# Kernel optimization log

Hardware: AMD Instinct MI355X
Metric: run time of the kernel (lower is better)

## Reference

```python
import jax, jax.numpy as jnp
import numpy as np

B, L, D, H = 2, 2048, 1024, 16
DH = D // H


def setup_inputs() -> dict:
    key = jax.random.key(0)
    ks = jax.random.split(key, 12)
    s = 0.02
    return {
        "q": jax.random.normal(ks[0], (B, L, D), jnp.float32),
        "k": jax.random.normal(ks[1], (B, L, D), jnp.float32),
        "v": jax.random.normal(ks[2], (B, L, D), jnp.float32),
        "pos_enc": jax.random.normal(ks[3], (L + 1, D), jnp.float32),
        "Wq": jax.random.normal(ks[4], (D, D), jnp.float32) * s,
        "bq": jnp.zeros((D,), jnp.float32),
        "Wk": jax.random.normal(ks[5], (D, D), jnp.float32) * s,
        "bk": jnp.zeros((D,), jnp.float32),
        "Wv": jax.random.normal(ks[6], (D, D), jnp.float32) * s,
        "bv": jnp.zeros((D,), jnp.float32),
        "Wo": jax.random.normal(ks[7], (D, D), jnp.float32) * s,
        "bo": jnp.zeros((D,), jnp.float32),
        "r_w_bias": jax.random.normal(ks[8], (H, 1, DH), jnp.float32) * s,
        "r_r_bias": jax.random.normal(ks[9], (H, 1, DH), jnp.float32) * s,
        "r_kernel": jax.random.normal(ks[10], (H, D, DH), jnp.float32) * s,
    }


def reference(q, k, v, pos_enc, Wq, bq, Wk, bk, Wv, bv, Wo, bo,
              r_w_bias, r_r_bias, r_kernel):
    b, lq, d = q.shape
    h, _, dh = r_w_bias.shape
    lk = k.shape[1]
    scale = dh ** -0.5

    # q/k/v projections, then split heads: [b, l, d] -> [b, h, l, dh]
    qh = (q @ Wq + bq).reshape(b, lq, h, dh).transpose(0, 2, 1, 3)
    kh = (k @ Wk + bk).reshape(b, lk, h, dh).transpose(0, 2, 1, 3)
    vh = (v @ Wv + bv).reshape(b, lk, h, dh).transpose(0, 2, 1, 3)

    # content scores with global content bias (Transformer-XL r_w_bias)
    scores = jnp.einsum('bhqd,bhkd->bhqk', qh + r_w_bias, kh) * scale

    # relative-position term: pos_enc [p, d] @ r_kernel [h, d, dh] -> [h, p, dh]
    pe = jnp.einsum('pd,hde->hpe', pos_enc, r_kernel)
    rel = jnp.einsum('bhqd,hpd->bhqp', qh + r_r_bias, pe) * scale  # [b,h,lq,p]
    p = rel.shape[-1]
    shift = 1 + (lq != lk)
    # rel-shift trick: reshape with swapped last two dims, drop first `shift`
    # rows, reshape back, keep first lk columns
    rel = rel.reshape(b, h, p, lq)[:, :, shift:, :]
    rel = rel.reshape(b, h, lq, p - shift)[..., :lk]
    scores = scores + rel

    # causal mask (key_cache is None path): subtract 1e7 on strict upper triangle
    causal_mask = jnp.triu(jnp.ones((lq, lk), dtype=bool), 1)
    scores = scores - causal_mask * 1e7

    out = jnp.einsum('bhqk,bhkd->bhqd', jax.nn.softmax(scores, axis=-1), vh)
    out = out.transpose(0, 2, 1, 3).reshape(b, lq, d)  # merge heads
    return out @ Wo + bo
```

## Files before the change

kernel.cpp:

```cpp
#include <hip/hip_runtime.h>
#include <hip/hip_bf16.h>

typedef __attribute__((ext_vector_type(8))) short bf16x8;
typedef __attribute__((ext_vector_type(4))) float f32x4;
typedef __attribute__((ext_vector_type(16))) float f32x16;
typedef unsigned short u16;
typedef unsigned int u32;

#define DEV static __device__ __forceinline__

DEV u16 f2us(float x) {
  __hip_bfloat16 h = __float2bfloat16(x);
  union { __hip_bfloat16 h; u16 u; } c; c.h = h; return c.u;
}
DEV float us2f(u16 u) {
  union { __hip_bfloat16 h; u16 u; } c; c.u = u;
  return __bfloat162float(c.h);
}
DEV f32x16 mfma32(bf16x8 a, bf16x8 b, f32x16 c) {
  return __builtin_amdgcn_mfma_f32_32x32x16_bf16(a, b, c, 0, 0, 0);
}
DEV void gl16(const u16* g, u16* l) {
  __builtin_amdgcn_global_load_lds(
      (const __attribute__((address_space(1))) unsigned int*)(g),
      (__attribute__((address_space(3))) unsigned int*)(l), 16, 0, 0);
}

constexpr int PE_ROWS = 2144;
constexpr int PE_M    = 2176;

constexpr size_t SZ_QKV  = (size_t)4096 * 1024 * 2;
constexpr size_t SZ_W    = (size_t)1024 * 1024 * 2;
constexpr size_t SZ_POSB = (size_t)PE_M * 1024 * 2;
constexpr size_t OFF_QB   = 0;
constexpr size_t OFF_KB   = OFF_QB  + SZ_QKV;
constexpr size_t OFF_VB   = OFF_KB  + SZ_QKV;
constexpr size_t OFF_WQT  = OFF_VB  + SZ_QKV;
constexpr size_t OFF_WKT  = OFF_WQT + SZ_W;
constexpr size_t OFF_WVT  = OFF_WKT + SZ_W;
constexpr size_t OFF_WOT  = OFF_WVT + SZ_W;
constexpr size_t OFF_RKT  = OFF_WOT + SZ_W;
constexpr size_t OFF_POSB = OFF_RKT + SZ_W;
constexpr size_t OFF_QW   = OFF_POSB + SZ_POSB;
constexpr size_t OFF_QR   = OFF_QW  + SZ_QKV;
constexpr size_t OFF_KH   = OFF_QR  + SZ_QKV;
constexpr size_t OFF_VT   = OFF_KH  + SZ_QKV;
constexpr size_t OFF_PEH  = OFF_VT  + SZ_QKV;
constexpr size_t OFF_ATTNB = OFF_QB;

__global__ __launch_bounds__(256)
void k_f2b4z(const float4* __restrict__ in, u16* __restrict__ out, int n4in, int n4tot) {
  int i = blockIdx.x * 256 + threadIdx.x;
  if (i >= n4tot) return;
  float4 v;
  if (i < n4in) v = in[i];
  else { v.x = v.y = v.z = v.w = 0.f; }
  ushort4 o;
  o.x = f2us(v.x); o.y = f2us(v.y); o.z = f2us(v.z); o.w = f2us(v.w);
  *reinterpret_cast<ushort4*>(out + (size_t)i * 4) = o;
}

__global__ __launch_bounds__(256)
void k_tconv(const float* __restrict__ in, u16* __restrict__ out) {
  __shared__ float t[32][33];
  const int kb0 = blockIdx.x * 32, nb0 = blockIdx.y * 32;
  const int tx = threadIdx.x & 31, ty = threadIdx.x >> 5;
#pragma unroll
  for (int r = 0; r < 32; r += 8)
    t[ty + r][tx] = in[(size_t)(kb0 + ty + r) * 1024 + nb0 + tx];
  __syncthreads();
#pragma unroll
  for (int r = 0; r < 32; r += 8)
    out[(size_t)(nb0 + ty + r) * 1024 + kb0 + tx] = f2us(t[tx][ty + r]);
}

__global__ __launch_bounds__(256)
void k_rkt(const float* __restrict__ rk, u16* __restrict__ out) {
  __shared__ float t[32][33];
  const int h = blockIdx.z;
  const int eb0 = blockIdx.x * 32, db0 = blockIdx.y * 32;
  const int tx = threadIdx.x & 31, ty = threadIdx.x >> 5;
#pragma unroll
  for (int r = 0; r < 32; r += 8)
    t[ty + r][tx] = rk[(size_t)h * 65536 + (size_t)(db0 + ty + r) * 64 + eb0 + tx];
  __syncthreads();
#pragma unroll
  for (int r = 0; r < 32; r += 8)
    out[(size_t)(h * 64 + eb0 + ty + r) * 1024 + db0 + tx] = f2us(t[tx][ty + r]);
}

struct ProjPtrs {
  const u16 *A0, *A1, *A2, *A3;
  const u16 *B0, *B1, *B2, *B3;
  const float *bias0, *bias1, *bias2;
  const float *rwb, *rrb;
  u16 *Qw, *Qr, *Kh, *Vt, *PEh;
};

__global__ __launch_bounds__(256)
void k_gemm_proj(ProjPtrs pp)
{
  const int z = blockIdx.z;
  if (z == 3 && blockIdx.y >= PE_M / 128) return;
  const u16* A  = (z == 0) ? pp.A0 : (z == 1) ? pp.A1 : (z == 2) ? pp.A2 : pp.A3;
  const u16* Bt = (z == 0) ? pp.B0 : (z == 1) ? pp.B1 : (z == 2) ? pp.B2 : pp.B3;

  __shared__ __attribute__((aligned(16))) u16 As[128 * 32];
  __shared__ __attribute__((aligned(16))) u16 Bs[128 * 32];
  const int tid  = threadIdx.x;
  const int lane = tid & 63;
  const int wave = tid >> 6;
  const int bm = blockIdx.y * 128;
  const int bn = blockIdx.x * 128;
  const int wr = (wave >> 1) * 64;
  const int wc = (wave & 1) * 64;
  const int fr = lane & 15;
  const int fk = (lane >> 4) * 8;

  f32x4 zero = {0.f, 0.f, 0.f, 0.f};
  f32x4 acc[4][4];
#pragma unroll
  for (int m = 0; m < 4; ++m)
#pragma unroll
    for (int n = 0; n < 4; ++n) acc[m][n] = zero;

  const int cA = wave * 2;
  const u16* gA = A  + (size_t)(bm + cA * 16 + (lane >> 2)) * 1024 + (lane & 3) * 8;
  const u16* gB = Bt + (size_t)(bn + cA * 16 + (lane >> 2)) * 1024 + (lane & 3) * 8;
  u16* lA = As + cA * 512;
  u16* lB = Bs + cA * 512;

  for (int k0 = 0; k0 < 1024; k0 += 32) {
    gl16(gA + k0, lA);
    gl16(gA + 16 * 1024 + k0, lA + 512);
    gl16(gB + k0, lB);
    gl16(gB + 16 * 1024 + k0, lB + 512);
    __syncthreads();
    bf16x8 af[4], bfv[4];
#pragma unroll
    for (int m = 0; m < 4; ++m) af[m]  = *(const bf16x8*)(&As[(wr + m * 16 + fr) * 32 + fk]);
#pragma unroll
    for (int n = 0; n < 4; ++n) bfv[n] = *(const bf16x8*)(&Bs[(wc + n * 16 + fr) * 32 + fk]);
#pragma unroll
    for (int m = 0; m < 4; ++m)
#pragma unroll
      for (int n = 0; n < 4; ++n)
        acc[m][n] = __builtin_amdgcn_mfma_f32_16x16x32_bf16(af[m], bfv[n], acc[m][n], 0, 0, 0);
    __syncthreads();
  }

#pragma unroll
  for (int m = 0; m < 4; ++m)
#pragma unroll
    for (int n = 0; n < 4; ++n)
#pragma unroll
      for (int r = 0; r < 4; ++r) {
        const int grow = bm + wr + m * 16 + (lane >> 4) * 4 + r;
        const int gcol = bn + wc + n * 16 + fr;
        float v = acc[m][n][r];
        const int b_ = grow >> 11, l_ = grow & 2047;
        const int h_ = gcol >> 6,  e_ = gcol & 63;
        if (z == 0) {
          v += pp.bias0[gcol];
          const size_t o = (((size_t)(b_ * 16 + h_) * 2048 + l_) << 6) + e_;
          pp.Qw[o] = f2us(v + pp.rwb[gcol]);
          pp.Qr[o] = f2us(v + pp.rrb[gcol]);
        } else if (z == 1) {
          v += pp.bias1[gcol];
          const size_t o = (((size_t)(b_ * 16 + h_) * 2048 + l_) << 6) + e_;
          pp.Kh[o] = f2us(v);
        } else if (z == 2) {
          v += pp.bias2[gcol];
          const size_t o = (((size_t)(b_ * 16 + h_) * 64 + e_) << 11) + l_;
          pp.Vt[o] = f2us(v);
        } else {
          if (grow < PE_ROWS) {
            const size_t o = ((size_t)h_ * PE_ROWS + grow) * 64 + e_;
            pp.PEh[o] = f2us(v);
          }
        }
      }
}

__global__ __launch_bounds__(256)
void k_gemm_o(const u16* __restrict__ A, const u16* __restrict__ Bt,
              const float* __restrict__ bias, float* __restrict__ outf)
{
  __shared__ __attribute__((aligned(16))) u16 As[128 * 32];
  __shared__ __attribute__((aligned(16))) u16 Bs[128 * 32];
  const int tid  = threadIdx.x;
  const int lane = tid & 63;
  const int wave = tid >> 6;
  const int bm = blockIdx.y * 128;
  const int bn = blockIdx.x * 128;
  const int wr = (wave >> 1) * 64;
  const int wc = (wave & 1) * 64;
  const int fr = lane & 15;
  const int fk = (lane >> 4) * 8;

  f32x4 zero = {0.f, 0.f, 0.f, 0.f};
  f32x4 acc[4][4];
#pragma unroll
  for (int m = 0; m < 4; ++m)
#pragma unroll
    for (int n = 0; n < 4; ++n) acc[m][n] = zero;

  const int cA = wave * 2;
  const u16* gA = A  + (size_t)(bm + cA * 16 + (lane >> 2)) * 1024 + (lane & 3) * 8;
  const u16* gB = Bt + (size_t)(bn + cA * 16 + (lane >> 2)) * 1024 + (lane & 3) * 8;
  u16* lA = As + cA * 512;
  u16* lB = Bs + cA * 512;

  for (int k0 = 0; k0 < 1024; k0 += 32) {
    gl16(gA + k0, lA);
    gl16(gA + 16 * 1024 + k0, lA + 512);
    gl16(gB + k0, lB);
    gl16(gB + 16 * 1024 + k0, lB + 512);
    __syncthreads();
    bf16x8 af[4], bfv[4];
#pragma unroll
    for (int m = 0; m < 4; ++m) af[m]  = *(const bf16x8*)(&As[(wr + m * 16 + fr) * 32 + fk]);
#pragma unroll
    for (int n = 0; n < 4; ++n) bfv[n] = *(const bf16x8*)(&Bs[(wc + n * 16 + fr) * 32 + fk]);
#pragma unroll
    for (int m = 0; m < 4; ++m)
#pragma unroll
      for (int n = 0; n < 4; ++n)
        acc[m][n] = __builtin_amdgcn_mfma_f32_16x16x32_bf16(af[m], bfv[n], acc[m][n], 0, 0, 0);
    __syncthreads();
  }

#pragma unroll
  for (int m = 0; m < 4; ++m)
#pragma unroll
    for (int n = 0; n < 4; ++n)
#pragma unroll
      for (int r = 0; r < 4; ++r) {
        const int grow = bm + wr + m * 16 + (lane >> 4) * 4 + r;
        const int gcol = bn + wc + n * 16 + fr;
        outf[(size_t)grow * 1024 + gcol] = acc[m][n][r] + bias[gcol];
      }
}

__global__ __launch_bounds__(256, 2)
void k_attn(const u16* __restrict__ Qw, const u16* __restrict__ Qr,
            const u16* __restrict__ Kh, const u16* __restrict__ Vt,
            const u16* __restrict__ PEh, u16* __restrict__ attnb)
{
  const int bid = blockIdx.x;
  const int xcd = bid & 7, slot = bid >> 3;
  const int jb = slot & 15, g = slot >> 4;
  const int hb = xcd + 8 * g;
  const int h = hb & 15, b = hb >> 4;
  const int wave = threadIdx.x >> 6, lane = threadIdx.x & 63;
  const int l31 = lane & 31, hi = lane >> 5;
  const int par = ((slot >> 5) ^ jb) & 1;
  const int tshort = (wave & 2) ? 2 * jb + 1 : 2 * jb;
  const int tlong  = (wave & 2) ? 62 - 2 * jb : 63 - 2 * jb;
  const int qt = ((wave & 1) ^ par) ? tlong : tshort;
  const int q0 = qt * 32;

  const u16* Qw_h = Qw + (size_t)hb * (2048 * 64);
  const u16* Qr_h = Qr + (size_t)hb * (2048 * 64);
  const u16* K_h  = Kh + (size_t)hb * (2048 * 64);
  const u16* V_h  = Vt + (size_t)hb * (64 * 2048);
  const u16* PE_h = PEh + (size_t)h * (PE_ROWS * 64);

  __shared__ float Elds_all[4][32][100];
  float (*Elds)[100] = Elds_all[wave];

  bf16x8 qwf[4], qrf[4];
#pragma unroll
  for (int kk = 0; kk < 4; ++kk) {
    qwf[kk] = *(const bf16x8*)(Qw_h + (size_t)(q0 + l31) * 64 + kk * 16 + hi * 8);
    qrf[kk] = *(const bf16x8*)(Qr_h + (size_t)(q0 + l31) * 64 + kk * 16 + hi * 8);
  }

  const int Jb0 = 2017 - q0;
  f32x16 carry = {};
#pragma unroll
  for (int kk = 0; kk < 4; ++kk) {
    bf16x8 pe = *(const bf16x8*)(PE_h + (size_t)(Jb0 + l31) * 64 + kk * 16 + hi * 8);
    carry = mfma32(pe, qrf[kk], carry);
  }

  f32x16 Oac[2] = {};
  float mrun = -1e30f, ls = 0.f;

  for (int c0 = 0; c0 <= q0 + 31; c0 += 64) {
    const int Jb = Jb0 + c0;
    bf16x8 pe1[4], pe2[4], kf0[4], kf1[4];
#pragma unroll
    for (int kk = 0; kk < 4; ++kk) {
      const int ko = kk * 16 + hi * 8;
      pe1[kk] = *(const bf16x8*)(PE_h + (size_t)(Jb + 32 + l31) * 64 + ko);
      pe2[kk] = *(const bf16x8*)(PE_h + (size_t)(Jb + 64 + l31) * 64 + ko);
      kf0[kk] = *(const bf16x8*)(K_h + (size_t)(c0 + l31) * 64 + ko);
      kf1[kk] = *(const bf16x8*)(K_h + (size_t)(c0 + 32 + l31) * 64 + ko);
    }
    bf16x8 vfr[2][2][2];
#pragma unroll
    for (int kt = 0; kt < 2; ++kt)
#pragma unroll
      for (int kvs = 0; kvs < 2; ++kvs)
#pragma unroll
        for (int dt = 0; dt < 2; ++dt)
          vfr[kt][kvs][dt] = *(const bf16x8*)(V_h + (size_t)(dt * 32 + l31) * 2048
                                              + c0 + kt * 32 + kvs * 16 + hi * 8);
#pragma unroll
    for (int g4 = 0; g4 < 4; ++g4) {
      float4 w4 = {carry[4 * g4], carry[4 * g4 + 1], carry[4 * g4 + 2], carry[4 * g4 + 3]};
      *(float4*)&Elds[l31][g4 * 8 + hi * 4] = w4;
    }
    {
      f32x16 e1 = {}, e2 = {};
#pragma unroll
      for (int kk = 0; kk < 4; ++kk) e1 = mfma32(pe1[kk], qrf[kk], e1);
#pragma unroll
      for (int kk = 0; kk < 4; ++kk) e2 = mfma32(pe2[kk], qrf[kk], e2);
#pragma unroll
      for (int g4 = 0; g4 < 4; ++g4) {
        float4 w4 = {e1[4 * g4], e1[4 * g4 + 1], e1[4 * g4 + 2], e1[4 * g4 + 3]};
        *(float4*)&Elds[l31][32 + g4 * 8 + hi * 4] = w4;
      }
#pragma unroll
      for (int g4 = 0; g4 < 4; ++g4) {
        float4 w4 = {e2[4 * g4], e2[4 * g4 + 1], e2[4 * g4 + 2], e2[4 * g4 + 3]};
        *(float4*)&Elds[l31][64 + g4 * 8 + hi * 4] = w4;
      }
      carry = e2;
    }
    f32x16 s0 = {}, s1 = {};
#pragma unroll
    for (int kk = 0; kk < 4; ++kk) s0 = mfma32(kf0[kk], qwf[kk], s0);
#pragma unroll
    for (int kk = 0; kk < 4; ++kk) s1 = mfma32(kf1[kk], qwf[kk], s1);
#pragma unroll
    for (int r = 0; r < 16; ++r) {
      const int pat = (r & 3) + 8 * (r >> 2) + 4 * hi;
      float e = Elds[l31][pat + 31 - l31];
      float x = (s0[r] + e) * 0.125f;
      if (c0 + pat > q0 + l31) x = -1e30f;
      s0[r] = x;
    }
#pragma unroll
    for (int r = 0; r < 16; ++r) {
      const int pat = (r & 3) + 8 * (r >> 2) + 4 * hi;
      float e = Elds[l31][32 + pat + 31 - l31];
      float x = (s1[r] + e) * 0.125f;
      if (c0 + 32 + pat > q0 + l31) x = -1e30f;
      s1[r] = x;
    }
    float mx = fmaxf(s0[0], s1[0]);
#pragma unroll
    for (int r = 1; r < 16; ++r) mx = fmaxf(mx, fmaxf(s0[r], s1[r]));
    mx = fmaxf(mx, __shfl_xor(mx, 32));
    const float mn = fmaxf(mrun, mx);
    const float al = __expf(mrun - mn);
    mrun = mn;

    float rsum = 0.f;
    u32 w0a[8], w1a[8];
#pragma unroll
    for (int g8 = 0; g8 < 8; ++g8) {
      float pa = __expf(s0[2 * g8] - mn);
      float pb = __expf(s0[2 * g8 + 1] - mn);
      u16 ua = f2us(pa), ub = f2us(pb);
      rsum += us2f(ua) + us2f(ub);
      w0a[g8] = (u32)ua | ((u32)ub << 16);
    }
#pragma unroll
    for (int g8 = 0; g8 < 8; ++g8) {
      float pa = __expf(s1[2 * g8] - mn);
      float pb = __expf(s1[2 * g8 + 1] - mn);
      u16 ua = f2us(pa), ub = f2us(pb);
      rsum += us2f(ua) + us2f(ub);
      w1a[g8] = (u32)ua | ((u32)ub << 16);
    }
    ls = ls * al + rsum + __shfl_xor(rsum, 32);
    Oac[0] *= al;
    Oac[1] *= al;

#define PV_KT(WARR, KT)                                                        \
    {                                                                          \
      _Pragma("unroll")                                                        \
      for (int kvs = 0; kvs < 2; ++kvs) {                                      \
        u32 snd0 = hi ? WARR[4 * kvs]     : WARR[4 * kvs + 2];                 \
        u32 snd1 = hi ? WARR[4 * kvs + 1] : WARR[4 * kvs + 3];                 \
        u32 r0 = (u32)__shfl_xor((int)snd0, 32);                               \
        u32 r1 = (u32)__shfl_xor((int)snd1, 32);                               \
        union { u32 u[4]; bf16x8 v; } pf;                                      \
        pf.u[0] = hi ? r0 : WARR[4 * kvs];                                     \
        pf.u[1] = hi ? r1 : WARR[4 * kvs + 1];                                 \
        pf.u[2] = hi ? WARR[4 * kvs + 2] : r0;                                 \
        pf.u[3] = hi ? WARR[4 * kvs + 3] : r1;                                 \
        _Pragma("unroll")                                                      \
        for (int dt = 0; dt < 2; ++dt)                                         \
          Oac[dt] = mfma32(vfr[KT][kvs][dt], pf.v, Oac[dt]);                   \
      }                                                                        \
    }
    PV_KT(w0a, 0)
    PV_KT(w1a, 1)
#undef PV_KT
  }

  const float invl = 1.f / ls;
  const size_t orow = ((size_t)(b * 2048 + q0 + l31)) * 1024 + h * 64;
#pragma unroll
  for (int dt = 0; dt < 2; ++dt)
#pragma unroll
    for (int g4 = 0; g4 < 4; ++g4) {
      ushort4 st;
      st.x = f2us(Oac[dt][4 * g4 + 0] * invl);
      st.y = f2us(Oac[dt][4 * g4 + 1] * invl);
      st.z = f2us(Oac[dt][4 * g4 + 2] * invl);
      st.w = f2us(Oac[dt][4 * g4 + 3] * invl);
      *(ushort4*)(attnb + orow + dt * 32 + g4 * 8 + hi * 4) = st;
    }
}

extern "C" void kernel_launch(void* const* d_in, const int* in_sizes, int n_in,
                              void* d_out, int out_size, void* d_ws, size_t ws_size,
                              hipStream_t stream)
{
  const float* q   = (const float*)d_in[0];
  const float* k   = (const float*)d_in[1];
  const float* v   = (const float*)d_in[2];
  const float* pos = (const float*)d_in[3];
  const float* Wq  = (const float*)d_in[4];
  const float* bq  = (const float*)d_in[5];
  const float* Wk  = (const float*)d_in[6];
  const float* bk  = (const float*)d_in[7];
  const float* Wv  = (const float*)d_in[8];
  const float* bv  = (const float*)d_in[9];
  const float* Wo  = (const float*)d_in[10];
  const float* bo  = (const float*)d_in[11];
  const float* rwb = (const float*)d_in[12];
  const float* rrb = (const float*)d_in[13];
  const float* rk  = (const float*)d_in[14];

  char* ws = (char*)d_ws;
  u16* qb    = (u16*)(ws + OFF_QB);
  u16* kb    = (u16*)(ws + OFF_KB);
  u16* vb    = (u16*)(ws + OFF_VB);
  u16* Wqt   = (u16*)(ws + OFF_WQT);
  u16* Wkt   = (u16*)(ws + OFF_WKT);
  u16* Wvt   = (u16*)(ws + OFF_WVT);
  u16* Wot   = (u16*)(ws + OFF_WOT);
  u16* Rkt   = (u16*)(ws + OFF_RKT);
  u16* posb  = (u16*)(ws + OFF_POSB);
  u16* Qw    = (u16*)(ws + OFF_QW);
  u16* Qr    = (u16*)(ws + OFF_QR);
  u16* Kh    = (u16*)(ws + OFF_KH);
  u16* Vt    = (u16*)(ws + OFF_VT);
  u16* PEh   = (u16*)(ws + OFF_PEH);
  u16* attnb = (u16*)(ws + OFF_ATTNB);
  float* outf = (float*)d_out;

  k_f2b4z<<<dim3(4096), 256, 0, stream>>>((const float4*)q, qb, 1048576, 1048576);
  k_f2b4z<<<dim3(4096), 256, 0, stream>>>((const float4*)k, kb, 1048576, 1048576);
  k_f2b4z<<<dim3(4096), 256, 0, stream>>>((const float4*)v, vb, 1048576, 1048576);
  k_f2b4z<<<dim3(2176), 256, 0, stream>>>((const float4*)pos, posb,
                                          (2049 * 1024) / 4, (PE_M * 1024) / 4);
  k_tconv<<<dim3(32, 32), 256, 0, stream>>>(Wq, Wqt);
  k_tconv<<<dim3(32, 32), 256, 0, stream>>>(Wk, Wkt);
  k_tconv<<<dim3(32, 32), 256, 0, stream>>>(Wv, Wvt);
  k_tconv<<<dim3(32, 32), 256, 0, stream>>>(Wo, Wot);
  k_rkt<<<dim3(2, 32, 16), 256, 0, stream>>>(rk, Rkt);

  ProjPtrs pp;
  pp.A0 = qb;  pp.A1 = kb;  pp.A2 = vb;  pp.A3 = posb;
  pp.B0 = Wqt; pp.B1 = Wkt; pp.B2 = Wvt; pp.B3 = Rkt;
  pp.bias0 = bq; pp.bias1 = bk; pp.bias2 = bv;
  pp.rwb = rwb; pp.rrb = rrb;
  pp.Qw = Qw; pp.Qr = Qr; pp.Kh = Kh; pp.Vt = Vt; pp.PEh = PEh;
  k_gemm_proj<<<dim3(8, 32, 4), 256, 0, stream>>>(pp);

  k_attn<<<dim3(512), 256, 0, stream>>>(Qw, Qr, Kh, Vt, PEh, attnb);

  k_gemm_o<<<dim3(8, 32), 256, 0, stream>>>(attnb, Wot, bo, outf);
}
```

Before: 266.6 us.

## Split attention KV range across waves, fold scale into Q, merge prep launches

Measured after the change: 305.1 us. +14.4%, slower.

```diff
diff --git a/kernel.cpp b/kernel.cpp
--- a/kernel.cpp
+++ b/kernel.cpp
@@ -20,6 +20,9 @@
 DEV f32x16 mfma32(bf16x8 a, bf16x8 b, f32x16 c) {
   return __builtin_amdgcn_mfma_f32_32x32x16_bf16(a, b, c, 0, 0, 0);
 }
+DEV u32 pkbf(float a, float b) {
+  return (u32)f2us(a) | ((u32)f2us(b) << 16);
+}
 DEV void gl16(const u16* g, u16* l) {
   __builtin_amdgcn_global_load_lds(
       (const __attribute__((address_space(1))) unsigned int*)(g),
@@ -28,6 +31,7 @@
 
 constexpr int PE_ROWS = 2144;
 constexpr int PE_M    = 2176;
+constexpr float QSCALE = 0.125f;
 
 constexpr size_t SZ_QKV  = (size_t)4096 * 1024 * 2;
 constexpr size_t SZ_W    = (size_t)1024 * 1024 * 2;
@@ -49,19 +53,34 @@
 constexpr size_t OFF_ATTNB = OFF_QB;
 
 __global__ __launch_bounds__(256)
-void k_f2b4z(const float4* __restrict__ in, u16* __restrict__ out, int n4in, int n4tot) {
-  int i = blockIdx.x * 256 + threadIdx.x;
+void k_f2b_all(const float4* __restrict__ q, const float4* __restrict__ k,
+               const float4* __restrict__ v, const float4* __restrict__ pos,
+               u16* __restrict__ qb, u16* __restrict__ kb,
+               u16* __restrict__ vb, u16* __restrict__ posb)
+{
+  const int bid = blockIdx.x;
+  const float4* src; u16* dst; int i; int n4in, n4tot;
+  if (bid < 4096)       { src = q;   dst = qb;   i = bid * 256 + threadIdx.x;           n4in = 1048576; n4tot = 1048576; }
+  else if (bid < 8192)  { src = k;   dst = kb;   i = (bid - 4096) * 256 + threadIdx.x;  n4in = 1048576; n4tot = 1048576; }
+  else if (bid < 12288) { src = v;   dst = vb;   i = (bid - 8192) * 256 + threadIdx.x;  n4in = 1048576; n4tot = 1048576; }
+  else                  { src = pos; dst = posb; i = (bid - 12288) * 256 + threadIdx.x; n4in = 524544;  n4tot = 557056; }
   if (i >= n4tot) return;
-  float4 v;
-  if (i < n4in) v = in[i];
-  else { v.x = v.y = v.z = v.w = 0.f; }
+  float4 val;
+  if (i < n4in) val = src[i];
+  else { val.x = val.y = val.z = val.w = 0.f; }
   ushort4 o;
-  o.x = f2us(v.x); o.y = f2us(v.y); o.z = f2us(v.z); o.w = f2us(v.w);
-  *reinterpret_cast<ushort4*>(out + (size_t)i * 4) = o;
-}
+  o.x = f2us(val.x); o.y = f2us(val.y); o.z = f2us(val.z); o.w = f2us(val.w);
+  *reinterpret_cast<ushort4*>(dst + (size_t)i * 4) = o;
+}
+
+struct TcPtrs { const float *i0, *i1, *i2, *i3; u16 *o0, *o1, *o2, *o3; };
 
 __global__ __launch_bounds__(256)
-void k_tconv(const float* __restrict__ in, u16* __restrict__ out) {
+void k_tconv4(TcPtrs tp)
+{
+  const int z = blockIdx.z;
+  const float* in = (z == 0) ? tp.i0 : (z == 1) ? tp.i1 : (z == 2) ? tp.i2 : tp.i3;
+  u16* out = (z == 0) ? tp.o0 : (z == 1) ? tp.o1 : (z == 2) ? tp.o2 : tp.o3;
   __shared__ float t[32][33];
   const int kb0 = blockIdx.x * 32, nb0 = blockIdx.y * 32;
   const int tx = threadIdx.x & 31, ty = threadIdx.x >> 5;
@@ -163,8 +182,8 @@
         if (z == 0) {
           v += pp.bias0[gcol];
           const size_t o = (((size_t)(b_ * 16 + h_) * 2048 + l_) << 6) + e_;
-          pp.Qw[o] = f2us(v + pp.rwb[gcol]);
-          pp.Qr[o] = f2us(v + pp.rrb[gcol]);
+          pp.Qw[o] = f2us((v + pp.rwb[gcol]) * QSCALE);
+          pp.Qr[o] = f2us((v + pp.rrb[gcol]) * QSCALE);
         } else if (z == 1) {
           v += pp.bias1[gcol];
           const size_t o = (((size_t)(b_ * 16 + h_) * 2048 + l_) << 6) + e_;
@@ -242,23 +261,22 @@
       }
 }
 
-__global__ __launch_bounds__(256, 2)
+__global__ __launch_bounds__(256, 4)
 void k_attn(const u16* __restrict__ Qw, const u16* __restrict__ Qr,
             const u16* __restrict__ Kh, const u16* __restrict__ Vt,
             const u16* __restrict__ PEh, u16* __restrict__ attnb)
 {
   const int bid = blockIdx.x;
-  const int xcd = bid & 7, slot = bid >> 3;
-  const int jb = slot & 15, g = slot >> 4;
+  const int xcd = bid & 7, s = bid >> 3;
+  const int p = s & 31, g = s >> 5;
   const int hb = xcd + 8 * g;
   const int h = hb & 15, b = hb >> 4;
   const int wave = threadIdx.x >> 6, lane = threadIdx.x & 63;
   const int l31 = lane & 31, hi = lane >> 5;
-  const int par = ((slot >> 5) ^ jb) & 1;
-  const int tshort = (wave & 2) ? 2 * jb + 1 : 2 * jb;
-  const int tlong  = (wave & 2) ? 62 - 2 * jb : 63 - 2 * jb;
-  const int qt = ((wave & 1) ^ par) ? tlong : tshort;
-  const int q0 = qt * 32;
+
+  const int qtL = 63 - p, qtS = p;
+  const int q0L = qtL * 32, q0S = qtS * 32;
+  const int nstL = qtL / 2 + 1;
 
   const u16* Qw_h = Qw + (size_t)hb * (2048 * 64);
   const u16* Qr_h = Qr + (size_t)hb * (2048 * 64);
@@ -266,157 +284,203 @@
   const u16* V_h  = Vt + (size_t)hb * (64 * 2048);
   const u16* PE_h = PEh + (size_t)h * (PE_ROWS * 64);
 
-  __shared__ float Elds_all[4][32][100];
-  float (*Elds)[100] = Elds_all[wave];
-
-  bf16x8 qwf[4], qrf[4];
-#pragma unroll
-  for (int kk = 0; kk < 4; ++kk) {
-    qwf[kk] = *(const bf16x8*)(Qw_h + (size_t)(q0 + l31) * 64 + kk * 16 + hi * 8);
-    qrf[kk] = *(const bf16x8*)(Qr_h + (size_t)(q0 + l31) * 64 + kk * 16 + hi * 8);
+  __shared__ __attribute__((aligned(16))) u16 Elds_all[4][32][100];
+  __shared__ float Obuf[32][66];
+  __shared__ float mlb[2][4][2][32];
+  u16 (*Ew)[100] = Elds_all[wave];
+
+  const int lo  = wave ? 9 + 8 * (wave - 1) : 0;
+  const int hiE = wave ? lo + 8 : 9;
+  const int la0 = lo,                      la1 = (hiE < nstL ? hiE : nstL);
+  const int lb0 = (lo - nstL > 0 ? lo - nstL : 0), lb1 = hiE - nstL;
+
+  f32x16 OacA[2] = {}, OacB[2] = {};
+  float mA = -1e30f, lA = 0.f, mB = -1e30f, lB = 0.f;
+
+  auto runseg = [&](int q0, int s0, int s1, f32x16* Oac, float& mrun, float& ls) {
+    if (s0 >= s1) return;
+    bf16x8 qwf[4], qrf[4];
+#pragma unroll
+    for (int kk = 0; kk < 4; ++kk) {
+      qwf[kk] = *(const bf16x8*)(Qw_h + (size_t)(q0 + l31) * 64 + kk * 16 + hi * 8);
+      qrf[kk] = *(const bf16x8*)(Qr_h + (size_t)(q0 + l31) * 64 + kk * 16 + hi * 8);
+    }
+    for (int st = s0; st < s1; ++st) {
+      const int c0 = st * 64;
+      const int Jb = 2048 + c0 - q0 - 31;
+      bf16x8 pef[3][4], kf[2][4];
+#pragma unroll
+      for (int kk = 0; kk < 4; ++kk) {
+        const int ko = kk * 16 + hi * 8;
+        pef[0][kk] = *(const bf16x8*)(PE_h + (size_t)(Jb + l31) * 64 + ko);
+        pef[1][kk] = *(const bf16x8*)(PE_h + (size_t)(Jb + 32 + l31) * 64 + ko);
+        pef[2][kk] = *(const bf16x8*)(PE_h + (size_t)(Jb + 64 + l31) * 64 + ko);
+        kf[0][kk]  = *(const bf16x8*)(K_h + (size_t)(c0 + l31) * 64 + ko);
+        kf[1][kk]  = *(const bf16x8*)(K_h + (size_t)(c0 + 32 + l31) * 64 + ko);
+      }
+#pragma unroll
+      for (int tau = 0; tau < 3; ++tau) {
+        f32x16 e = {};
+#pragma unroll
+        for (int kk = 0; kk < 4; ++kk) e = mfma32(pef[tau][kk], qrf[kk], e);
+#pragma unroll
+        for (int g4 = 0; g4 < 4; ++g4) {
+          uint2 w2;
+          w2.x = pkbf(e[4 * g4 + 0], e[4 * g4 + 1]);
+          w2.y = pkbf(e[4 * g4 + 2], e[4 * g4 + 3]);
+          *(uint2*)(&Ew[l31][tau * 32 + 8 * g4 + 4 * hi]) = w2;
+        }
+      }
+      f32x16 s0v = {}, s1v = {};
+#pragma unroll
+      for (int kk = 0; kk < 4; ++kk) s0v = mfma32(kf[0][kk], qwf[kk], s0v);
+#pragma unroll
+      for (int kk = 0; kk < 4; ++kk) s1v = mfma32(kf[1][kk], qwf[kk], s1v);
+      bf16x8 vfr[2][2][2];
+#pragma unroll
+      for (int kt = 0; kt < 2; ++kt)
+#pragma unroll
+        for (int kvs = 0; kvs < 2; ++kvs)
+#pragma unroll
+          for (int dt = 0; dt < 2; ++dt)
+            vfr[kt][kvs][dt] = *(const bf16x8*)(V_h + (size_t)(dt * 32 + l31) * 2048
+                                                + c0 + kt * 32 + kvs * 16 + hi * 8);
+#pragma unroll
+      for (int r = 0; r < 16; ++r) {
+        const int pat = (r & 3) + 8 * (r >> 2) + 4 * hi;
+        float x = s0v[r] + us2f(Ew[l31][pat + 31 - l31]);
+        if (c0 + pat > q0 + l31) x = -1e30f;
+        s0v[r] = x;
+      }
+#pragma unroll
+      for (int r = 0; r < 16; ++r) {
+        const int pat = (r & 3) + 8 * (r >> 2) + 4 * hi;
+        float x = s1v[r] + us2f(Ew[l31][32 + pat + 31 - l31]);
+        if (c0 + 32 + pat > q0 + l31) x = -1e30f;
+        s1v[r] = x;
+      }
+      float mx = fmaxf(s0v[0], s1v[0]);
+#pragma unroll
+      for (int r = 1; r < 16; ++r) mx = fmaxf(mx, fmaxf(s0v[r], s1v[r]));
+      mx = fmaxf(mx, __shfl_xor(mx, 32));
+      const float mn = fmaxf(mrun, mx);
+      const float al = __expf(mrun - mn);
+      mrun = mn;
+
+      float rsum = 0.f;
+      u32 w0a[8], w1a[8];
+#pragma unroll
+      for (int g8 = 0; g8 < 8; ++g8) {
+        float pa = __expf(s0v[2 * g8] - mn);
+        float pb = __expf(s0v[2 * g8 + 1] - mn);
+        u16 ua = f2us(pa), ub = f2us(pb);
+        rsum += us2f(ua) + us2f(ub);
+        w0a[g8] = (u32)ua | ((u32)ub << 16);
+      }
+#pragma unroll
+      for (int g8 = 0; g8 < 8; ++g8) {
+        float pa = __expf(s1v[2 * g8] - mn);
+        float pb = __expf(s1v[2 * g8 + 1] - mn);
+        u16 ua = f2us(pa), ub = f2us(pb);
+        rsum += us2f(ua) + us2f(ub);
+        w1a[g8] = (u32)ua | ((u32)ub << 16);
+      }
+      ls = ls * al + rsum + __shfl_xor(rsum, 32);
+      Oac[0] *= al;
+      Oac[1] *= al;
+
+#define PV_KT(WARR, KT)                                                        \
+      {                                                                        \
+        _Pragma("unroll")                                                      \
+        for (int kvs = 0; kvs < 2; ++kvs) {                                    \
+          u32 snd0 = hi ? WARR[4 * kvs]     : WARR[4 * kvs + 2];               \
+          u32 snd1 = hi ? WARR[4 * kvs + 1] : WARR[4 * kvs + 3];               \
+          u32 r0 = (u32)__shfl_xor((int)snd0, 32);                             \
+          u32 r1 = (u32)__shfl_xor((int)snd1, 32);                             \
+          union { u32 u[4]; bf16x8 v; } pf;                                    \
+          pf.u[0] = hi ? r0 : WARR[4 * kvs];                                   \
+          pf.u[1] = hi ? r1 : WARR[4 * kvs + 1];                               \
+          pf.u[2] = hi ? WARR[4 * kvs + 2] : r0;                               \
+          pf.u[3] = hi ? WARR[4 * kvs + 3] : r1;                               \
+          _Pragma("unroll")                                                    \
+          for (int dt = 0; dt < 2; ++dt)                                       \
+            Oac[dt] = mfma32(vfr[KT][kvs][dt], pf.v, Oac[dt]);                 \
+        }                                                                      \
+      }
+      PV_KT(w0a, 0)
+      PV_KT(w1a, 1)
+#undef PV_KT
+    }
+  };
+
+  runseg(q0L, la0, la1, OacA, mA, lA);
+  runseg(q0S, lb0, lb1, OacB, mB, lB);
+
+  __syncthreads();
+  if (hi == 0) {
+    mlb[0][wave][0][l31] = mA; mlb[0][wave][1][l31] = lA;
+    mlb[1][wave][0][l31] = mB; mlb[1][wave][1][l31] = lB;
   }
-
-  const int Jb0 = 2017 - q0;
-  f32x16 carry = {};
-#pragma unroll
-  for (int kk = 0; kk < 4; ++kk) {
-    bf16x8 pe = *(const bf16x8*)(PE_h + (size_t)(Jb0 + l31) * 64 + kk * 16 + hi * 8);
-    carry = mfma32(pe, qrf[kk], carry);
-  }
-
-  f32x16 Oac[2] = {};
-  float mrun = -1e30f, ls = 0.f;
-
-  for (int c0 = 0; c0 <= q0 + 31; c0 += 64) {
-    const int Jb = Jb0 + c0;
-    bf16x8 pe1[4], pe2[4], kf0[4], kf1[4];
-#pragma unroll
-    for (int kk = 0; kk < 4; ++kk) {
-      const int ko = kk * 16 + hi * 8;
-      pe1[kk] = *(const bf16x8*)(PE_h + (size_t)(Jb + 32 + l31) * 64 + ko);
-      pe2[kk] = *(const bf16x8*)(PE_h + (size_t)(Jb + 64 + l31) * 64 + ko);
-      kf0[kk] = *(const bf16x8*)(K_h + (size_t)(c0 + l31) * 64 + ko);
-      kf1[kk] = *(const bf16x8*)(K_h + (size_t)(c0 + 32 + l31) * 64 + ko);
+  __syncthreads();
+
+  auto obWrite = [&](f32x16* Oac, float scl, bool acc) {
+#pragma unroll
+    for (int dt = 0; dt < 2; ++dt)
+#pragma unroll
+      for (int g4 = 0; g4 < 4; ++g4) {
+        float* pb = &Obuf[l31][dt * 32 + 8 * g4 + 4 * hi];
+        float v0 = Oac[dt][4 * g4 + 0] * scl, v1 = Oac[dt][4 * g4 + 1] * scl;
+        float v2 = Oac[dt][4 * g4 + 2] * scl, v3 = Oac[dt][4 * g4 + 3] * scl;
+        if (acc) {
+          float2 t0 = *(float2*)pb;       t0.x += v0; t0.y += v1; *(float2*)pb = t0;
+          float2 t1 = *(float2*)(pb + 2); t1.x += v2; t1.y += v3; *(float2*)(pb + 2) = t1;
+        } else {
+          float2 t0; t0.x = v0; t0.y = v1; *(float2*)pb = t0;
+          float2 t1; t1.x = v2; t1.y = v3; *(float2*)(pb + 2) = t1;
+        }
+      }
+  };
+  auto finalize = [&](int q0T, int tIdx, float mstT) {
+    float lst = 0.f;
+#pragma unroll
+    for (int w = 0; w < 4; ++w)
+      lst += mlb[tIdx][w][1][l31] * __expf(mlb[tIdx][w][0][l31] - mstT);
+    const float inv = 1.f / lst;
+    const size_t orow = ((size_t)(b * 2048 + q0T + l31)) * 1024 + h * 64 + hi * 32;
+#pragma unroll
+    for (int j4 = 0; j4 < 32; j4 += 4) {
+      float2 t0 = *(float2*)&Obuf[l31][hi * 32 + j4];
+      float2 t1 = *(float2*)&Obuf[l31][hi * 32 + j4 + 2];
+      ushort4 st;
+      st.x = f2us(t0.x * inv); st.y = f2us(t0.y * inv);
+      st.z = f2us(t1.x * inv); st.w = f2us(t1.y * inv);
+      *(ushort4*)(attnb + orow + j4) = st;
     }
-    bf16x8 vfr[2][2][2];
-#pragma unroll
-    for (int kt = 0; kt < 2; ++kt)
-#pragma unroll
-      for (int kvs = 0; kvs < 2; ++kvs)
-#pragma unroll
-        for (int dt = 0; dt < 2; ++dt)
-          vfr[kt][kvs][dt] = *(const bf16x8*)(V_h + (size_t)(dt * 32 + l31) * 2048
-                                              + c0 + kt * 32 + kvs * 16 + hi * 8);
-#pragma unroll
-    for (int g4 = 0; g4 < 4; ++g4) {
-      float4 w4 = {carry[4 * g4], carry[4 * g4 + 1], carry[4 * g4 + 2], carry[4 * g4 + 3]};
-      *(float4*)&Elds[l31][g4 * 8 + hi * 4] = w4;
-    }
-    {
-      f32x16 e1 = {}, e2 = {};
-#pragma unroll
-      for (int kk = 0; kk < 4; ++kk) e1 = mfma32(pe1[kk], qrf[kk], e1);
-#pragma unroll
-      for (int kk = 0; kk < 4; ++kk) e2 = mfma32(pe2[kk], qrf[kk], e2);
-#pragma unroll
-      for (int g4 = 0; g4 < 4; ++g4) {
-        float4 w4 = {e1[4 * g4], e1[4 * g4 + 1], e1[4 * g4 + 2], e1[4 * g4 + 3]};
-        *(float4*)&Elds[l31][32 + g4 * 8 + hi * 4] = w4;
-      }
-#pragma unroll
-      for (int g4 = 0; g4 < 4; ++g4) {
-        float4 w4 = {e2[4 * g4], e2[4 * g4 + 1], e2[4 * g4 + 2], e2[4 * g4 + 3]};
-        *(float4*)&Elds[l31][64 + g4 * 8 + hi * 4] = w4;
-      }
-      carry = e2;
-    }
-    f32x16 s0 = {}, s1 = {};
-#pragma unroll
-    for (int kk = 0; kk < 4; ++kk) s0 = mfma32(kf0[kk], qwf[kk], s0);
-#pragma unroll
-    for (int kk = 0; kk < 4; ++kk) s1 = mfma32(kf1[kk], qwf[kk], s1);
-#pragma unroll
-    for (int r = 0; r < 16; ++r) {
-      const int pat = (r & 3) + 8 * (r >> 2) + 4 * hi;
-      float e = Elds[l31][pat + 31 - l31];
-      float x = (s0[r] + e) * 0.125f;
-      if (c0 + pat > q0 + l31) x = -1e30f;
-      s0[r] = x;
-    }
-#pragma unroll
-    for (int r = 0; r < 16; ++r) {
-      const int pat = (r & 3) + 8 * (r >> 2) + 4 * hi;
-      float e = Elds[l31][32 + pat + 31 - l31];
-      float x = (s1[r] + e) * 0.125f;
-      if (c0 + 32 + pat > q0 + l31) x = -1e30f;
-      s1[r] = x;
-    }
-    float mx = fmaxf(s0[0], s1[0]);
-#pragma unroll
-    for (int r = 1; r < 16; ++r) mx = fmaxf(mx, fmaxf(s0[r], s1[r]));
-    mx = fmaxf(mx, __shfl_xor(mx, 32));
-    const float mn = fmaxf(mrun, mx);
-    const float al = __expf(mrun - mn);
-    mrun = mn;
-
-    float rsum = 0.f;
-    u32 w0a[8], w1a[8];
-#pragma unroll
-    for (int g8 = 0; g8 < 8; ++g8) {
-      float pa = __expf(s0[2 * g8] - mn);
-      float pb = __expf(s0[2 * g8 + 1] - mn);
-      u16 ua = f2us(pa), ub = f2us(pb);
-      rsum += us2f(ua) + us2f(ub);
-      w0a[g8] = (u32)ua | ((u32)ub << 16);
-    }
-#pragma unroll
-    for (int g8 = 0; g8 < 8; ++g8) {
-      float pa = __expf(s1[2 * g8] - mn);
-      float pb = __expf(s1[2 * g8 + 1] - mn);
-      u16 ua = f2us(pa), ub = f2us(pb);
-      rsum += us2f(ua) + us2f(ub);
-      w1a[g8] = (u32)ua | ((u32)ub << 16);
-    }
-    ls = ls * al + rsum + __shfl_xor(rsum, 32);
-    Oac[0] *= al;
-    Oac[1] *= al;
-
-#define PV_KT(WARR, KT)                                                        \
-    {                                                                          \
-      _Pragma("unroll")                                                        \
-      for (int kvs = 0; kvs < 2; ++kvs) {                                      \
-        u32 snd0 = hi ? WARR[4 * kvs]     : WARR[4 * kvs + 2];                 \
-        u32 snd1 = hi ? WARR[4 * kvs + 1] : WARR[4 * kvs + 3];                 \
-        u32 r0 = (u32)__shfl_xor((int)snd0, 32);                               \
-        u32 r1 = (u32)__shfl_xor((int)snd1, 32);                               \
-        union { u32 u[4]; bf16x8 v; } pf;                                      \
-        pf.u[0] = hi ? r0 : WARR[4 * kvs];                                     \
-        pf.u[1] = hi ? r1 : WARR[4 * kvs + 1];                                 \
-        pf.u[2] = hi ? WARR[4 * kvs + 2] : r0;                                 \
-        pf.u[3] = hi ? WARR[4 * kvs + 3] : r1;                                 \
-        _Pragma("unroll")                                                      \
-        for (int dt = 0; dt < 2; ++dt)                                         \
-          Oac[dt] = mfma32(vfr[KT][kvs][dt], pf.v, Oac[dt]);                   \
-      }                                                                        \
-    }
-    PV_KT(w0a, 0)
-    PV_KT(w1a, 1)
-#undef PV_KT
-  }
-
-  const float invl = 1.f / ls;
-  const size_t orow = ((size_t)(b * 2048 + q0 + l31)) * 1024 + h * 64;
-#pragma unroll
-  for (int dt = 0; dt < 2; ++dt)
-#pragma unroll
-    for (int g4 = 0; g4 < 4; ++g4) {
-      ushort4 st;
-      st.x = f2us(Oac[dt][4 * g4 + 0] * invl);
-      st.y = f2us(Oac[dt][4 * g4 + 1] * invl);
-      st.z = f2us(Oac[dt][4 * g4 + 2] * invl);
-      st.w = f2us(Oac[dt][4 * g4 + 3] * invl);
-      *(ushort4*)(attnb + orow + dt * 32 + g4 * 8 + hi * 4) = st;
-    }
+  };
+
+  const bool hasL = la1 > la0;
+  const bool hasS = lb1 > lb0;
+  float mstL = fmaxf(fmaxf(mlb[0][0][0][l31], mlb[0][1][0][l31]),
+                     fmaxf(mlb[0][2][0][l31], mlb[0][3][0][l31]));
+  float sclL = __expf(mA - mstL);
+  if (wave == 0) obWrite(OacA, sclL, false);
+  __syncthreads();
+  if (wave == 1) obWrite(OacA, sclL, true);
+  __syncthreads();
+  if (wave == 2 && hasL) obWrite(OacA, sclL, true);
+  __syncthreads();
+  if (wave == 3 && hasL) obWrite(OacA, sclL, true);
+  __syncthreads();
+  if (wave == 0) finalize(q0L, 0, mstL);
+  __syncthreads();
+  const int sfw = (nstL < 25) ? 2 : 3;
+  float mstS = fmaxf(mlb[1][2][0][l31], mlb[1][3][0][l31]);
+  float sclS = __expf(mB - mstS);
+  if (wave == sfw) obWrite(OacB, sclS, false);
+  __syncthreads();
+  if (wave == 3 && nstL < 25 && hasS) obWrite(OacB, sclS, true);
+  __syncthreads();
+  if (wave == 1) finalize(q0S, 1, mstS);
 }
 
 extern "C" void kernel_launch(void* const* d_in, const int* in_sizes, int n_in,
@@ -457,15 +521,13 @@
   u16* attnb = (u16*)(ws + OFF_ATTNB);
   float* outf = (float*)d_out;
 
-  k_f2b4z<<<dim3(4096), 256, 0, stream>>>((const float4*)q, qb, 1048576, 1048576);
-  k_f2b4z<<<dim3(4096), 256, 0, stream>>>((const float4*)k, kb, 1048576, 1048576);
-  k_f2b4z<<<dim3(4096), 256, 0, stream>>>((const float4*)v, vb, 1048576, 1048576);
-  k_f2b4z<<<dim3(2176), 256, 0, stream>>>((const float4*)pos, posb,
-                                          (2049 * 1024) / 4, (PE_M * 1024) / 4);
-  k_tconv<<<dim3(32, 32), 256, 0, stream>>>(Wq, Wqt);
-  k_tconv<<<dim3(32, 32), 256, 0, stream>>>(Wk, Wkt);
-  k_tconv<<<dim3(32, 32), 256, 0, stream>>>(Wv, Wvt);
-  k_tconv<<<dim3(32, 32), 256, 0, stream>>>(Wo, Wot);
+  k_f2b_all<<<dim3(14464), 256, 0, stream>>>((const float4*)q, (const float4*)k,
+                                             (const float4*)v, (const float4*)pos,
+                                             qb, kb, vb, posb);
+  TcPtrs tp;
+  tp.i0 = Wq; tp.i1 = Wk; tp.i2 = Wv; tp.i3 = Wo;
+  tp.o0 = Wqt; tp.o1 = Wkt; tp.o2 = Wvt; tp.o3 = Wot;
+  k_tconv4<<<dim3(32, 32, 4), 256, 0, stream>>>(tp);
   k_rkt<<<dim3(2, 32, 16), 256, 0, stream>>>(rk, Rkt);
 
   ProjPtrs pp;
@@ -476,7 +538,7 @@
   pp.Qw = Qw; pp.Qr = Qr; pp.Kh = Kh; pp.Vt = Vt; pp.PEh = PEh;
   k_gemm_proj<<<dim3(8, 32, 4), 256, 0, stream>>>(pp);
 
-  k_attn<<<dim3(512), 256, 0, stream>>>(Qw, Qr, Kh, Vt, PEh, attnb);
+  k_attn<<<dim3(1024), 256, 0, stream>>>(Qw, Qr, Kh, Vt, PEh, attnb);
 
   k_gemm_o<<<dim3(8, 32), 256, 0, stream>>>(attnb, Wot, bo, outf);
 }
```
